# Optimization experiments

Hardware: AMD Instinct MI355X
Metric: run time of the kernel (lower is better)

The kernel has to match this reference:

```python
import jax, jax.numpy as jnp
import numpy as np

N, E, K, F, R = 100000, 200000, 16, 32, 2
EPS = 1e-5

def setup_inputs() -> dict:
    key = jax.random.key(0)
    ks = jax.random.split(key, 32)
    inp = {}
    inp['x'] = jax.random.normal(ks[0], (N, F), jnp.float32)
    inp['y'] = jax.random.normal(ks[1], (E, F), jnp.float32)
    inp['deg_g'] = jax.random.uniform(ks[2], (N, 1), jnp.float32)
    inp['deg_lg'] = jax.random.uniform(ks[3], (E, 1), jnp.float32)
    inp['t_g'] = jax.random.randint(ks[4], (N, K), 0, N)
    inp['tt_g'] = jax.random.randint(ks[5], (N, K), 0, N)
    inp['t_lg'] = jax.random.randint(ks[6], (E, K), 0, E)
    inp['tt_lg'] = jax.random.randint(ks[7], (E, K), 0, E)
    inp['dst'] = jax.random.randint(ks[8], (E,), 0, N)
    inp['pm_pd'] = jax.random.randint(ks[9], (E,), 0, N)
    i = [10]
    def mk(shape):
        a = jax.random.normal(ks[i[0]], shape, jnp.float32) * 0.1
        i[0] += 1
        return a
    for nm in ['theta_x', 'theta_deg', 'theta_y', 'gamma_y', 'gamma_deg', 'gamma_x']:
        inp[nm + '_w'] = mk((F, F)); inp[nm + '_b'] = mk((F,))
    inp['theta_r_w'] = mk((R, F, F)); inp['theta_r_b'] = mk((R, F))
    inp['gamma_r_w'] = mk((R, F, F)); inp['gamma_r_b'] = mk((R, F))
    inp['bn_x_w'] = jnp.ones((F,), jnp.float32); inp['bn_x_b'] = jnp.zeros((F,), jnp.float32)
    inp['bn_y_w'] = jnp.ones((F,), jnp.float32); inp['bn_y_b'] = jnp.zeros((F,), jnp.float32)
    return inp

def _lin(a, w, b):
    return a @ w + b

def _bn(a, w, b):
    # BatchNorm1d in training mode: biased batch stats
    m = a.mean(axis=0)
    v = a.var(axis=0)
    return (a - m) / jnp.sqrt(v + EPS) * w + b

def _aggregate(z, t, tt):
    # per-node gather+sum over neighbor index lists (t: radius-0, tt: radius-1)
    return jnp.stack([z[t].sum(axis=1), z[tt].sum(axis=1)])  # [R, M, F]

def reference(x, y, deg_g, deg_lg, t_g, tt_g, t_lg, tt_lg, dst, pm_pd,
              theta_x_w, theta_x_b, theta_deg_w, theta_deg_b, theta_y_w, theta_y_b,
              gamma_y_w, gamma_y_b, gamma_deg_w, gamma_deg_b, gamma_x_w, gamma_x_b,
              theta_r_w, theta_r_b, gamma_r_w, gamma_r_b,
              bn_x_w, bn_x_b, bn_y_w, bn_y_b):
    n = F // 2
    pmpd_x = x[pm_pd]                                   # [E, F] embedding gather
    zs = _aggregate(x, t_g, tt_g)                        # [R, N, F]
    sum_x = jnp.einsum('rnf,rfo->no', zs, theta_r_w) + theta_r_b.sum(axis=0)
    pmpd_y = jax.ops.segment_sum(y, dst, num_segments=x.shape[0])  # copy_edge + sum
    xo = (_lin(x, theta_x_w, theta_x_b)
          + _lin(deg_g * x, theta_deg_w, theta_deg_b)
          + sum_x
          + _lin(pmpd_y, theta_y_w, theta_y_b))
    xo = jnp.concatenate([xo[:, :n], jax.nn.relu(xo[:, n:])], axis=1)
    xo = _bn(xo, bn_x_w, bn_x_b)
    zy = _aggregate(y, t_lg, tt_lg)                      # [R, E, F]
    sum_y = jnp.einsum('ref,rfo->eo', zy, gamma_r_w) + gamma_r_b.sum(axis=0)
    yo = (_lin(y, gamma_y_w, gamma_y_b)
          + _lin(deg_lg * y, gamma_deg_w, gamma_deg_b)
          + sum_y
          + _lin(pmpd_x, gamma_x_w, gamma_x_b))
    yo = jnp.concatenate([yo[:, :n], jax.nn.relu(yo[:, n:])], axis=1)
    yo = _bn(yo, bn_y_w, bn_y_b)
    return xo, yo
```

## Files before the change

### kernel.cpp

```cpp
#include <hip/hip_runtime.h>

#define NN 100000
#define NE 200000
#define MT (NN + NE)

typedef unsigned short u16;
typedef __attribute__((ext_vector_type(8))) short bf16x8;
typedef __attribute__((ext_vector_type(4))) float f32x4;

__device__ __forceinline__ float bf2f(u16 u) {
    union { unsigned int i; float f; } v; v.i = ((unsigned int)u) << 16; return v.f;
}
__device__ __forceinline__ u16 f2bf(float f) {
    union { unsigned int i; float f; } v; v.f = f;
    unsigned int r = v.i + 0x7fffu + ((v.i >> 16) & 1u);
    return (u16)(r >> 16);
}
__device__ __forceinline__ void unpack2(unsigned int u, float& lo, float& hi) {
    union { unsigned int i; float f; } a, b;
    a.i = u << 16; b.i = u & 0xffff0000u;
    lo = a.f; hi = b.f;
}
__device__ __forceinline__ unsigned int pack2(float a, float b) {
    return (unsigned int)f2bf(a) | ((unsigned int)f2bf(b) << 16);
}
__device__ __forceinline__ float loadf(const void* p, size_t i, int f32) {
    return f32 ? ((const float*)p)[i] : bf2f(((const u16*)p)[i]);
}

__global__ void detect_kernel(const unsigned int* __restrict__ x, int* flag) {
    __shared__ int cnt;
    if (threadIdx.x == 0) cnt = 0;
    __syncthreads();
    int bad = 0;
    for (int i = threadIdx.x; i < 1024; i += 256) {
        unsigned int e = (x[i] >> 7) & 0xFF;
        if (e == 0xFF || (e > 0 && (e < 107 || e > 134))) bad++;
    }
    atomicAdd(&cnt, bad);
    __syncthreads();
    if (threadIdx.x == 0) *flag = (cnt > 256) ? 1 : 0;
}

__global__ __launch_bounds__(256) void prep_kernel(
    const void* txw, const void* tdw, const void* tyw,
    const void* gyw, const void* gdw, const void* gxw,
    const void* trw, const void* grw,
    const void* txb, const void* tdb, const void* tyb,
    const void* gyb, const void* gdb, const void* gxb,
    const void* trb, const void* grb,
    u16* Bfx, u16* Bfy, float* bx, float* by, const int* flagp)
{
    int f32 = *flagp;
    int t = blockIdx.x * 256 + threadIdx.x;
    if (t < 10240) {
        int side = t / 5120;
        int e = t - side * 5120;
        int b = e >> 9, lane = (e >> 3) & 63, j = e & 7;
        int m = b >> 1;
        int k = ((lane >> 4) << 3) + j;
        int f = ((b & 1) << 4) + (lane & 15);
        size_t idx = (size_t)k * 32 + f;
        float v;
        if (side == 0) {
            v = (m == 0) ? loadf(txw, idx, f32) : (m == 1) ? loadf(tdw, idx, f32)
              : (m == 2) ? loadf(trw, idx, f32) : (m == 3) ? loadf(trw, 1024 + idx, f32)
              : loadf(gxw, idx, f32);
            Bfx[e] = f2bf(v);
        } else {
            v = (m == 0) ? loadf(gyw, idx, f32) : (m == 1) ? loadf(gdw, idx, f32)
              : (m == 2) ? loadf(grw, idx, f32) : (m == 3) ? loadf(grw, 1024 + idx, f32)
              : loadf(tyw, idx, f32);
            Bfy[e] = f2bf(v);
        }
    } else if (t < 10304) {
        int f = t - 10240;
        if (f < 32) {
            bx[f] = loadf(txb, f, f32) + loadf(tdb, f, f32) + loadf(tyb, f, f32)
                  + loadf(trb, f, f32) + loadf(trb, 32 + f, f32);
        } else {
            f -= 32;
            by[f] = loadf(gyb, f, f32) + loadf(gdb, f, f32) + loadf(gxb, f, f32)
                  + loadf(grb, f, f32) + loadf(grb, 32 + f, f32);
        }
    }
}

__global__ __launch_bounds__(256, 4) void gemm2(
    const void* __restrict__ x, const void* __restrict__ y,
    const u16* __restrict__ Bfx, const u16* __restrict__ Bfy,
    const float* __restrict__ bx, const float* __restrict__ by,
    const void* __restrict__ deg_g, const void* __restrict__ deg_lg,
    const int* __restrict__ dst,
    u16* __restrict__ Xself, u16* __restrict__ Xt,
    u16* __restrict__ Xtt,   u16* __restrict__ Xaux,
    u16* __restrict__ Yself, u16* __restrict__ Yt, u16* __restrict__ Ytt,
    float* __restrict__ xacc, const int* __restrict__ flagp)
{
    int f32 = *flagp;
    int lane = threadIdx.x & 63;
    int wib  = threadIdx.x >> 6;
    bool is_y = (blockIdx.x >= 1563);
    int wid = (is_y ? (int)blockIdx.x - 1563 : (int)blockIdx.x) * 4 + wib;
    int nwaves = is_y ? 12500 : 6250;
    if (wid >= nwaves) return;
    int r0 = wid * 16;

    const void* feat = is_y ? y : x;
    const u16* Bf   = is_y ? Bfy : Bfx;
    const float* bias = is_y ? by : bx;
    const void* deg  = is_y ? deg_lg : deg_g;

    union { u16 s[8]; bf16x8 v; } au;
    {
        size_t eoff = (size_t)(r0 + (lane & 15)) * 32 + ((lane >> 4) << 3);
        if (f32) {
            const float4* fp = (const float4*)((const float*)feat + eoff);
            float4 A0 = fp[0], A1 = fp[1];
            au.s[0] = f2bf(A0.x); au.s[1] = f2bf(A0.y);
            au.s[2] = f2bf(A0.z); au.s[3] = f2bf(A0.w);
            au.s[4] = f2bf(A1.x); au.s[5] = f2bf(A1.y);
            au.s[6] = f2bf(A1.z); au.s[7] = f2bf(A1.w);
        } else {
            au.v = *(const bf16x8*)((const u16*)feat + eoff);
        }
    }
    f32x4 acc[10];
    const u16* bp = Bf + lane * 8;
#pragma unroll
    for (int b = 0; b < 10; ++b) {
        bf16x8 bfr = *(const bf16x8*)(bp + b * 512);
        f32x4 z = {0.f, 0.f, 0.f, 0.f};
        acc[b] = __builtin_amdgcn_mfma_f32_16x16x32_bf16(au.v, bfr, z, 0, 0, 0);
    }

    int n = lane & 15, quad = lane >> 4;
    int rowb = r0 + quad * 4;
    float bl = bias[n], bh = bias[16 + n];

#pragma unroll
    for (int i = 0; i < 4; ++i) {
        float dgi = loadf(deg, rowb + i, f32);
        size_t ro = (size_t)(rowb + i) * 32;
        u16 s_lo = f2bf(acc[0][i] + dgi * acc[2][i] + bl);
        u16 s_hi = f2bf(acc[1][i] + dgi * acc[3][i] + bh);
        if (!is_y) {
            Xself[ro + n]      = s_lo;
            Xself[ro + 16 + n] = s_hi;
            Xt[ro + n]         = f2bf(acc[4][i]);
            Xt[ro + 16 + n]    = f2bf(acc[5][i]);
            Xtt[ro + n]        = f2bf(acc[6][i]);
            Xtt[ro + 16 + n]   = f2bf(acc[7][i]);
            Xaux[ro + n]       = f2bf(acc[8][i]);
            Xaux[ro + 16 + n]  = f2bf(acc[9][i]);
        } else {
            Yself[ro + n]      = s_lo;
            Yself[ro + 16 + n] = s_hi;
            Yt[ro + n]         = f2bf(acc[4][i]);
            Yt[ro + 16 + n]    = f2bf(acc[5][i]);
            Ytt[ro + n]        = f2bf(acc[6][i]);
            Ytt[ro + 16 + n]   = f2bf(acc[7][i]);
            int d = dst[rowb + i];
            float* p = xacc + (size_t)d * 32;
            atomicAdd(p + n,      acc[8][i]);
            atomicAdd(p + 16 + n, acc[9][i]);
        }
    }
}

__global__ __launch_bounds__(256) void gather_fused(
    const u16* __restrict__ Xself, const u16* __restrict__ Xt,
    const u16* __restrict__ Xtt,   const u16* __restrict__ Xaux,
    const u16* __restrict__ Yself, const u16* __restrict__ Yt,
    const u16* __restrict__ Ytt,
    const float* __restrict__ xacc,
    const int* __restrict__ t_g, const int* __restrict__ tt_g,
    const int* __restrict__ t_lg, const int* __restrict__ tt_lg,
    const int* __restrict__ pm_pd,
    float* __restrict__ xpre, u16* __restrict__ ypre,
    float* __restrict__ stats)
{
    __shared__ int s_t[1024];
    __shared__ int s_tt[1024];
    __shared__ float s_sum[32];
    __shared__ float s_sq[32];
    bool is_y = (blockIdx.x >= 1563);
    int M = is_y ? NE : NN;
    const u16 *Self, *T, *TT;
    const int *tl, *ttl;
    if (is_y) { Self = Yself; T = Yt; TT = Ytt; tl = t_lg; ttl = tt_lg; }
    else      { Self = Xself; T = Xt; TT = Xtt; tl = t_g;  ttl = tt_g; }
    float* ss = stats + (is_y ? 64 : 0);

    if (threadIdx.x < 32) { s_sum[threadIdx.x] = 0.f; s_sq[threadIdx.x] = 0.f; }
    int row0 = (is_y ? (int)blockIdx.x - 1563 : (int)blockIdx.x) * 64;
    int lim = (M - row0) * 16;
    for (int i = threadIdx.x; i < 1024; i += 256) {
        s_t[i]  = (i < lim) ? tl[row0 * 16 + i]  : 0;
        s_tt[i] = (i < lim) ? ttl[row0 * 16 + i] : 0;
    }
    __syncthreads();

    int lr = threadIdx.x >> 2, q = threadIdx.x & 3;
    int r = row0 + lr;
    bool act = r < M;
    int rc = act ? r : row0;

    float a[8];
    {
        uint4 u = *(const uint4*)(Self + (size_t)rc * 32 + q * 8);
        unpack2(u.x, a[0], a[1]); unpack2(u.y, a[2], a[3]);
        unpack2(u.z, a[4], a[5]); unpack2(u.w, a[6], a[7]);
    }
    const int* il = &s_t[lr * 16];
    const int* ill = &s_tt[lr * 16];
#pragma unroll
    for (int batch = 0; batch < 2; ++batch) {
        uint4 g[8];
#pragma unroll
        for (int j = 0; j < 8; ++j)
            g[j] = *(const uint4*)(T + (size_t)il[batch * 8 + j] * 32 + q * 8);
#pragma unroll
        for (int j = 0; j < 8; ++j) {
            float e0, e1, e2, e3, e4, e5, e6, e7;
            unpack2(g[j].x, e0, e1); unpack2(g[j].y, e2, e3);
            unpack2(g[j].z, e4, e5); unpack2(g[j].w, e6, e7);
            a[0] += e0; a[1] += e1; a[2] += e2; a[3] += e3;
            a[4] += e4; a[5] += e5; a[6] += e6; a[7] += e7;
        }
    }
#pragma unroll
    for (int batch = 0; batch < 2; ++batch) {
        uint4 g[8];
#pragma unroll
        for (int j = 0; j < 8; ++j)
            g[j] = *(const uint4*)(TT + (size_t)ill[batch * 8 + j] * 32 + q * 8);
#pragma unroll
        for (int j = 0; j < 8; ++j) {
            float e0, e1, e2, e3, e4, e5, e6, e7;
            unpack2(g[j].x, e0, e1); unpack2(g[j].y, e2, e3);
            unpack2(g[j].z, e4, e5); unpack2(g[j].w, e6, e7);
            a[0] += e0; a[1] += e1; a[2] += e2; a[3] += e3;
            a[4] += e4; a[5] += e5; a[6] += e6; a[7] += e7;
        }
    }
    if (!is_y) {
        float4 b0 = *(const float4*)(xacc + (size_t)rc * 32 + q * 8);
        float4 b1 = *(const float4*)(xacc + (size_t)rc * 32 + q * 8 + 4);
        a[0] += b0.x; a[1] += b0.y; a[2] += b0.z; a[3] += b0.w;
        a[4] += b1.x; a[5] += b1.y; a[6] += b1.z; a[7] += b1.w;
    } else {
        int ai = pm_pd[rc];
        uint4 g = *(const uint4*)(Xaux + (size_t)ai * 32 + q * 8);
        float e0, e1, e2, e3, e4, e5, e6, e7;
        unpack2(g.x, e0, e1); unpack2(g.y, e2, e3);
        unpack2(g.z, e4, e5); unpack2(g.w, e6, e7);
        a[0] += e0; a[1] += e1; a[2] += e2; a[3] += e3;
        a[4] += e4; a[5] += e5; a[6] += e6; a[7] += e7;
    }
    if (q >= 2) {
#pragma unroll
        for (int i = 0; i < 8; ++i) a[i] = fmaxf(a[i], 0.f);
    }
    if (act) {
        if (!is_y) {
            float4 o0, o1;
            o0.x = a[0]; o0.y = a[1]; o0.z = a[2]; o0.w = a[3];
            o1.x = a[4]; o1.y = a[5]; o1.z = a[6]; o1.w = a[7];
            *(float4*)(xpre + (size_t)r * 32 + q * 8) = o0;
            *(float4*)(xpre + (size_t)r * 32 + q * 8 + 4) = o1;
        } else {
            uint4 o;
            o.x = pack2(a[0], a[1]); o.y = pack2(a[2], a[3]);
            o.z = pack2(a[4], a[5]); o.w = pack2(a[6], a[7]);
            *(uint4*)(ypre + (size_t)r * 32 + q * 8) = o;
        }
    } else {
#pragma unroll
        for (int i = 0; i < 8; ++i) a[i] = 0.f;
    }
#pragma unroll
    for (int i = 0; i < 8; ++i) {
        atomicAdd(&s_sum[q * 8 + i], a[i]);
        atomicAdd(&s_sq[q * 8 + i], a[i] * a[i]);
    }
    __syncthreads();
    if (threadIdx.x < 32) {
        atomicAdd(&ss[threadIdx.x], s_sum[threadIdx.x]);
        atomicAdd(&ss[32 + threadIdx.x], s_sq[threadIdx.x]);
    }
}

__global__ void finalize_stats(
    const float* stats,
    const void* bnxw, const void* bnxb, const void* bnyw, const void* bnyb,
    float* scsh, const int* flagp)
{
    int f32 = *flagp;
    int f = threadIdx.x;
    if (f < 32) {
        float m = stats[f] / (float)NN;
        float var = stats[32 + f] / (float)NN - m * m;
        float inv = rsqrtf(var + 1e-5f);
        float sc = loadf(bnxw, f, f32) * inv;
        scsh[f] = sc; scsh[32 + f] = loadf(bnxb, f, f32) - m * sc;
    } else if (f < 64) {
        int g = f - 32;
        float m = stats[64 + g] / (float)NE;
        float var = stats[96 + g] / (float)NE - m * m;
        float inv = rsqrtf(var + 1e-5f);
        float sc = loadf(bnyw, g, f32) * inv;
        scsh[64 + g] = sc; scsh[96 + g] = loadf(bnyb, g, f32) - m * sc;
    }
}

__global__ __launch_bounds__(256) void apply_bn(
    const float* __restrict__ xpre, const u16* __restrict__ ypre,
    const float* __restrict__ scsh, void* __restrict__ out,
    const int* __restrict__ flagp)
{
    int f32 = *flagp;
    int tid = blockIdx.x * 256 + threadIdx.x;
    if (tid >= MT * 8) return;
    int fq = (tid & 7) * 4;
    const float* sc;
    float4 v;
    if (tid < NN * 8) {
        v = ((const float4*)xpre)[tid];
        sc = scsh;
    } else {
        size_t off = (size_t)tid * 4 - (size_t)NN * 32;
        ushort4 u = *(const ushort4*)(ypre + off);
        v.x = bf2f(u.x); v.y = bf2f(u.y); v.z = bf2f(u.z); v.w = bf2f(u.w);
        sc = scsh + 64;
    }
    float o0 = v.x * sc[fq + 0] + sc[32 + fq + 0];
    float o1 = v.y * sc[fq + 1] + sc[32 + fq + 1];
    float o2 = v.z * sc[fq + 2] + sc[32 + fq + 2];
    float o3 = v.w * sc[fq + 3] + sc[32 + fq + 3];
    if (f32) {
        float4 o; o.x = o0; o.y = o1; o.z = o2; o.w = o3;
        ((float4*)out)[tid] = o;
    } else {
        ushort4 o; o.x = f2bf(o0); o.y = f2bf(o1); o.z = f2bf(o2); o.w = f2bf(o3);
        ((ushort4*)out)[tid] = o;
    }
}

extern "C" void kernel_launch(void* const* d_in, const int* in_sizes, int n_in,
                              void* d_out, int out_size, void* d_ws, size_t ws_size,
                              hipStream_t stream)
{
    const void* x      = d_in[0];
    const void* y      = d_in[1];
    const void* deg_g  = d_in[2];
    const void* deg_lg = d_in[3];
    const int* t_g   = (const int*)d_in[4];
    const int* tt_g  = (const int*)d_in[5];
    const int* t_lg  = (const int*)d_in[6];
    const int* tt_lg = (const int*)d_in[7];
    const int* dst   = (const int*)d_in[8];
    const int* pm_pd = (const int*)d_in[9];

    char* ws = (char*)d_ws;
    int*   flag = (int*)ws;
    u16* Bfx   = (u16*)(ws + 256);
    u16* Bfy   = Bfx + 5120;
    float* bx  = (float*)(ws + 24576);
    float* by  = bx + 32;
    float* stats = by + 32;
    float* scsh  = stats + 128;
    u16* Xself = (u16*)(ws + 65536);
    u16* Xt    = Xself + (size_t)NN * 32;
    u16* Xtt   = Xt    + (size_t)NN * 32;
    u16* Xaux  = Xtt   + (size_t)NN * 32;
    u16* Yself = Xaux  + (size_t)NN * 32;
    u16* Yt    = Yself + (size_t)NE * 32;
    u16* Ytt   = Yt    + (size_t)NE * 32;
    float* xacc = (float*)(Ytt + (size_t)NE * 32);
    u16* ypre = (u16*)(xacc + (size_t)NN * 32);

    hipMemsetAsync(stats, 0, 256 * sizeof(float), stream);
    hipMemsetAsync(xacc, 0, (size_t)NN * 32 * sizeof(float), stream);

    detect_kernel<<<1, 256, 0, stream>>>((const unsigned int*)x, flag);
    prep_kernel<<<41, 256, 0, stream>>>(
        d_in[10], d_in[12], d_in[14], d_in[16], d_in[18], d_in[20],
        d_in[22], d_in[24],
        d_in[11], d_in[13], d_in[15], d_in[17], d_in[19], d_in[21],
        d_in[23], d_in[25],
        Bfx, Bfy, bx, by, flag);
    gemm2<<<4688, 256, 0, stream>>>(x, y, Bfx, Bfy, bx, by, deg_g, deg_lg, dst,
                                    Xself, Xt, Xtt, Xaux, Yself, Yt, Ytt,
                                    xacc, flag);
    gather_fused<<<4688, 256, 0, stream>>>(Xself, Xt, Xtt, Xaux, Yself, Yt, Ytt,
                                           xacc, t_g, tt_g, t_lg, tt_lg, pm_pd,
                                           xacc, ypre, stats);
    finalize_stats<<<1, 64, 0, stream>>>(stats, d_in[26], d_in[27], d_in[28],
                                         d_in[29], scsh, flag);
    apply_bn<<<9375, 256, 0, stream>>>(xacc, ypre, scsh, d_out, flag);
}
```

Measured before the change: 418.2 us.

## Aggregate raw features before the GEMM instead of after the per-row projections

The old code projected every row through all weight matrices first and then gathered the projected T/TT/aux tables. The new code converts x and y to bf16 once, gathers and sums raw neighbour features, and applies the weights with MFMA after aggregation. It then fuses the projection, bias, ReLU and BN-stat accumulation into one kernel per side, with the y side run first so its atomics into xacc finish before the x side reads them. This removes the seven intermediate projected tables and most of their traffic. In exchange, the neighbour sums are rounded to bf16 before the MFMA, which can change precision, and the gathers now sit inside the GEMM kernel.

```diff
diff --git a/kernel.cpp b/kernel.cpp
--- a/kernel.cpp
+++ b/kernel.cpp
@@ -26,6 +26,13 @@
 }
 __device__ __forceinline__ float loadf(const void* p, size_t i, int f32) {
     return f32 ? ((const float*)p)[i] : bf2f(((const u16*)p)[i]);
+}
+__device__ __forceinline__ void acc8(float a[8], uint4 g) {
+    float e0, e1, e2, e3, e4, e5, e6, e7;
+    unpack2(g.x, e0, e1); unpack2(g.y, e2, e3);
+    unpack2(g.z, e4, e5); unpack2(g.w, e6, e7);
+    a[0] += e0; a[1] += e1; a[2] += e2; a[3] += e3;
+    a[4] += e4; a[5] += e5; a[6] += e6; a[7] += e7;
 }
 
 __global__ void detect_kernel(const unsigned int* __restrict__ x, int* flag) {
@@ -53,26 +60,26 @@
 {
     int f32 = *flagp;
     int t = blockIdx.x * 256 + threadIdx.x;
-    if (t < 10240) {
-        int side = t / 5120;
-        int e = t - side * 5120;
+    if (t < 4096) {
+        int b = t >> 9, lane = (t >> 3) & 63, j = t & 7;
+        int m = b >> 1;
+        int k = ((lane >> 4) << 3) + j;
+        int f = ((b & 1) << 4) + (lane & 15);
+        size_t idx = (size_t)k * 32 + f;
+        float v = (m == 0) ? loadf(txw, idx, f32) : (m == 1) ? loadf(tdw, idx, f32)
+                : (m == 2) ? loadf(trw, idx, f32) : loadf(trw, 1024 + idx, f32);
+        Bfx[t] = f2bf(v);
+    } else if (t < 10240) {
+        int e = t - 4096;
         int b = e >> 9, lane = (e >> 3) & 63, j = e & 7;
         int m = b >> 1;
         int k = ((lane >> 4) << 3) + j;
         int f = ((b & 1) << 4) + (lane & 15);
         size_t idx = (size_t)k * 32 + f;
-        float v;
-        if (side == 0) {
-            v = (m == 0) ? loadf(txw, idx, f32) : (m == 1) ? loadf(tdw, idx, f32)
-              : (m == 2) ? loadf(trw, idx, f32) : (m == 3) ? loadf(trw, 1024 + idx, f32)
-              : loadf(gxw, idx, f32);
-            Bfx[e] = f2bf(v);
-        } else {
-            v = (m == 0) ? loadf(gyw, idx, f32) : (m == 1) ? loadf(gdw, idx, f32)
-              : (m == 2) ? loadf(grw, idx, f32) : (m == 3) ? loadf(grw, 1024 + idx, f32)
-              : loadf(tyw, idx, f32);
-            Bfy[e] = f2bf(v);
-        }
+        float v = (m == 0) ? loadf(gyw, idx, f32) : (m == 1) ? loadf(gdw, idx, f32)
+                : (m == 2) ? loadf(grw, idx, f32) : (m == 3) ? loadf(grw, 1024 + idx, f32)
+                : (m == 4) ? loadf(gxw, idx, f32) : loadf(tyw, idx, f32);
+        Bfy[e] = f2bf(v);
     } else if (t < 10304) {
         int f = t - 10240;
         if (f < 32) {
@@ -86,206 +93,164 @@
     }
 }
 
-__global__ __launch_bounds__(256, 4) void gemm2(
+__global__ __launch_bounds__(256) void convert_kernel(
     const void* __restrict__ x, const void* __restrict__ y,
-    const u16* __restrict__ Bfx, const u16* __restrict__ Bfy,
-    const float* __restrict__ bx, const float* __restrict__ by,
-    const void* __restrict__ deg_g, const void* __restrict__ deg_lg,
-    const int* __restrict__ dst,
-    u16* __restrict__ Xself, u16* __restrict__ Xt,
-    u16* __restrict__ Xtt,   u16* __restrict__ Xaux,
-    u16* __restrict__ Yself, u16* __restrict__ Yt, u16* __restrict__ Ytt,
-    float* __restrict__ xacc, const int* __restrict__ flagp)
-{
-    int f32 = *flagp;
-    int lane = threadIdx.x & 63;
-    int wib  = threadIdx.x >> 6;
-    bool is_y = (blockIdx.x >= 1563);
-    int wid = (is_y ? (int)blockIdx.x - 1563 : (int)blockIdx.x) * 4 + wib;
-    int nwaves = is_y ? 12500 : 6250;
-    if (wid >= nwaves) return;
-    int r0 = wid * 16;
-
-    const void* feat = is_y ? y : x;
-    const u16* Bf   = is_y ? Bfy : Bfx;
-    const float* bias = is_y ? by : bx;
-    const void* deg  = is_y ? deg_lg : deg_g;
-
-    union { u16 s[8]; bf16x8 v; } au;
-    {
-        size_t eoff = (size_t)(r0 + (lane & 15)) * 32 + ((lane >> 4) << 3);
+    u16* __restrict__ xb, u16* __restrict__ yb, const int* __restrict__ flagp)
+{
+    int f32 = *flagp;
+    int t = blockIdx.x * 256 + threadIdx.x;
+    if (t < NN * 4) {
+        int r = t >> 2, q = t & 3;
+        uint4 o;
         if (f32) {
-            const float4* fp = (const float4*)((const float*)feat + eoff);
-            float4 A0 = fp[0], A1 = fp[1];
-            au.s[0] = f2bf(A0.x); au.s[1] = f2bf(A0.y);
-            au.s[2] = f2bf(A0.z); au.s[3] = f2bf(A0.w);
-            au.s[4] = f2bf(A1.x); au.s[5] = f2bf(A1.y);
-            au.s[6] = f2bf(A1.z); au.s[7] = f2bf(A1.w);
+            const float4* fp = (const float4*)((const float*)x + (size_t)r * 32 + q * 8);
+            float4 v0 = fp[0], v1 = fp[1];
+            o.x = pack2(v0.x, v0.y); o.y = pack2(v0.z, v0.w);
+            o.z = pack2(v1.x, v1.y); o.w = pack2(v1.z, v1.w);
         } else {
-            au.v = *(const bf16x8*)((const u16*)feat + eoff);
-        }
-    }
-    f32x4 acc[10];
-    const u16* bp = Bf + lane * 8;
-#pragma unroll
-    for (int b = 0; b < 10; ++b) {
-        bf16x8 bfr = *(const bf16x8*)(bp + b * 512);
-        f32x4 z = {0.f, 0.f, 0.f, 0.f};
-        acc[b] = __builtin_amdgcn_mfma_f32_16x16x32_bf16(au.v, bfr, z, 0, 0, 0);
-    }
-
-    int n = lane & 15, quad = lane >> 4;
-    int rowb = r0 + quad * 4;
-    float bl = bias[n], bh = bias[16 + n];
-
-#pragma unroll
-    for (int i = 0; i < 4; ++i) {
-        float dgi = loadf(deg, rowb + i, f32);
-        size_t ro = (size_t)(rowb + i) * 32;
-        u16 s_lo = f2bf(acc[0][i] + dgi * acc[2][i] + bl);
-        u16 s_hi = f2bf(acc[1][i] + dgi * acc[3][i] + bh);
-        if (!is_y) {
-            Xself[ro + n]      = s_lo;
-            Xself[ro + 16 + n] = s_hi;
-            Xt[ro + n]         = f2bf(acc[4][i]);
-            Xt[ro + 16 + n]    = f2bf(acc[5][i]);
-            Xtt[ro + n]        = f2bf(acc[6][i]);
-            Xtt[ro + 16 + n]   = f2bf(acc[7][i]);
-            Xaux[ro + n]       = f2bf(acc[8][i]);
-            Xaux[ro + 16 + n]  = f2bf(acc[9][i]);
+            o = *(const uint4*)((const u16*)x + (size_t)r * 32 + q * 8);
+        }
+        *(uint4*)(xb + (size_t)r * 32 + q * 8) = o;
+    } else if (t < MT * 4) {
+        int t2 = t - NN * 4;
+        int r = t2 >> 2, q = t2 & 3;
+        uint4 o;
+        if (f32) {
+            const float4* fp = (const float4*)((const float*)y + (size_t)r * 32 + q * 8);
+            float4 v0 = fp[0], v1 = fp[1];
+            o.x = pack2(v0.x, v0.y); o.y = pack2(v0.z, v0.w);
+            o.z = pack2(v1.x, v1.y); o.w = pack2(v1.z, v1.w);
         } else {
-            Yself[ro + n]      = s_lo;
-            Yself[ro + 16 + n] = s_hi;
-            Yt[ro + n]         = f2bf(acc[4][i]);
-            Yt[ro + 16 + n]    = f2bf(acc[5][i]);
-            Ytt[ro + n]        = f2bf(acc[6][i]);
-            Ytt[ro + 16 + n]   = f2bf(acc[7][i]);
-            int d = dst[rowb + i];
-            float* p = xacc + (size_t)d * 32;
-            atomicAdd(p + n,      acc[8][i]);
-            atomicAdd(p + 16 + n, acc[9][i]);
-        }
-    }
-}
-
-__global__ __launch_bounds__(256) void gather_fused(
-    const u16* __restrict__ Xself, const u16* __restrict__ Xt,
-    const u16* __restrict__ Xtt,   const u16* __restrict__ Xaux,
-    const u16* __restrict__ Yself, const u16* __restrict__ Yt,
-    const u16* __restrict__ Ytt,
-    const float* __restrict__ xacc,
-    const int* __restrict__ t_g, const int* __restrict__ tt_g,
-    const int* __restrict__ t_lg, const int* __restrict__ tt_lg,
-    const int* __restrict__ pm_pd,
-    float* __restrict__ xpre, u16* __restrict__ ypre,
-    float* __restrict__ stats)
+            o = *(const uint4*)((const u16*)y + (size_t)r * 32 + q * 8);
+        }
+        *(uint4*)(yb + (size_t)r * 32 + q * 8) = o;
+    }
+}
+
+template<int IS_Y>
+__global__ __launch_bounds__(256, 3) void fused_side(
+    const u16* __restrict__ xb, const u16* __restrict__ yb,
+    float* xacc,
+    const u16* __restrict__ Bf, const float* __restrict__ bias,
+    const void* __restrict__ deg,
+    const int* __restrict__ tl, const int* __restrict__ ttl,
+    const int* __restrict__ pm_pd, const int* __restrict__ dst,
+    float* xpre, u16* __restrict__ ypre,
+    float* __restrict__ stats, const int* __restrict__ flagp)
 {
     __shared__ int s_t[1024];
     __shared__ int s_tt[1024];
     __shared__ float s_sum[32];
     __shared__ float s_sq[32];
-    bool is_y = (blockIdx.x >= 1563);
-    int M = is_y ? NE : NN;
-    const u16 *Self, *T, *TT;
-    const int *tl, *ttl;
-    if (is_y) { Self = Yself; T = Yt; TT = Ytt; tl = t_lg; ttl = tt_lg; }
-    else      { Self = Xself; T = Xt; TT = Xtt; tl = t_g;  ttl = tt_g; }
-    float* ss = stats + (is_y ? 64 : 0);
-
+    const int M = IS_Y ? NE : NN;
+    int f32 = *flagp;
+    int row0 = (int)blockIdx.x * 64;
     if (threadIdx.x < 32) { s_sum[threadIdx.x] = 0.f; s_sq[threadIdx.x] = 0.f; }
-    int row0 = (is_y ? (int)blockIdx.x - 1563 : (int)blockIdx.x) * 64;
     int lim = (M - row0) * 16;
     for (int i = threadIdx.x; i < 1024; i += 256) {
-        s_t[i]  = (i < lim) ? tl[row0 * 16 + i]  : 0;
-        s_tt[i] = (i < lim) ? ttl[row0 * 16 + i] : 0;
+        s_t[i]  = (i < lim) ? tl[(size_t)row0 * 16 + i]  : 0;
+        s_tt[i] = (i < lim) ? ttl[(size_t)row0 * 16 + i] : 0;
     }
     __syncthreads();
-
-    int lr = threadIdx.x >> 2, q = threadIdx.x & 3;
-    int r = row0 + lr;
-    bool act = r < M;
-    int rc = act ? r : row0;
-
-    float a[8];
-    {
-        uint4 u = *(const uint4*)(Self + (size_t)rc * 32 + q * 8);
-        unpack2(u.x, a[0], a[1]); unpack2(u.y, a[2], a[3]);
-        unpack2(u.z, a[4], a[5]); unpack2(u.w, a[6], a[7]);
-    }
-    const int* il = &s_t[lr * 16];
-    const int* ill = &s_tt[lr * 16];
-#pragma unroll
-    for (int batch = 0; batch < 2; ++batch) {
-        uint4 g[8];
+    int lane = threadIdx.x & 63, wib = threadIdx.x >> 6;
+    int r0 = row0 + wib * 16;
+    if (r0 + 16 <= M) {
+        const u16* tab = IS_Y ? yb : xb;
+        int m = lane & 15, q = lane >> 4;
+        int gr = r0 + m;
+        const int* il  = &s_t[(wib * 16 + m) * 16];
+        const int* ill = &s_tt[(wib * 16 + m) * 16];
+
+        bf16x8 selfv = *(const bf16x8*)(tab + (size_t)gr * 32 + q * 8);
+        union { u16 s[8]; bf16x8 v; } pm;
+        if (IS_Y) {
+            int ai = pm_pd[gr];
+            pm.v = *(const bf16x8*)(xb + (size_t)ai * 32 + q * 8);
+        }
+
+        float aT[8]  = {0.f, 0.f, 0.f, 0.f, 0.f, 0.f, 0.f, 0.f};
+        float aTT[8] = {0.f, 0.f, 0.f, 0.f, 0.f, 0.f, 0.f, 0.f};
+        uint4 ga[8], gb[8];
 #pragma unroll
         for (int j = 0; j < 8; ++j)
-            g[j] = *(const uint4*)(T + (size_t)il[batch * 8 + j] * 32 + q * 8);
-#pragma unroll
-        for (int j = 0; j < 8; ++j) {
-            float e0, e1, e2, e3, e4, e5, e6, e7;
-            unpack2(g[j].x, e0, e1); unpack2(g[j].y, e2, e3);
-            unpack2(g[j].z, e4, e5); unpack2(g[j].w, e6, e7);
-            a[0] += e0; a[1] += e1; a[2] += e2; a[3] += e3;
-            a[4] += e4; a[5] += e5; a[6] += e6; a[7] += e7;
-        }
-    }
-#pragma unroll
-    for (int batch = 0; batch < 2; ++batch) {
-        uint4 g[8];
+            ga[j] = *(const uint4*)(tab + (size_t)il[j] * 32 + q * 8);
 #pragma unroll
         for (int j = 0; j < 8; ++j)
-            g[j] = *(const uint4*)(TT + (size_t)ill[batch * 8 + j] * 32 + q * 8);
-#pragma unroll
-        for (int j = 0; j < 8; ++j) {
-            float e0, e1, e2, e3, e4, e5, e6, e7;
-            unpack2(g[j].x, e0, e1); unpack2(g[j].y, e2, e3);
-            unpack2(g[j].z, e4, e5); unpack2(g[j].w, e6, e7);
-            a[0] += e0; a[1] += e1; a[2] += e2; a[3] += e3;
-            a[4] += e4; a[5] += e5; a[6] += e6; a[7] += e7;
-        }
-    }
-    if (!is_y) {
-        float4 b0 = *(const float4*)(xacc + (size_t)rc * 32 + q * 8);
-        float4 b1 = *(const float4*)(xacc + (size_t)rc * 32 + q * 8 + 4);
-        a[0] += b0.x; a[1] += b0.y; a[2] += b0.z; a[3] += b0.w;
-        a[4] += b1.x; a[5] += b1.y; a[6] += b1.z; a[7] += b1.w;
-    } else {
-        int ai = pm_pd[rc];
-        uint4 g = *(const uint4*)(Xaux + (size_t)ai * 32 + q * 8);
-        float e0, e1, e2, e3, e4, e5, e6, e7;
-        unpack2(g.x, e0, e1); unpack2(g.y, e2, e3);
-        unpack2(g.z, e4, e5); unpack2(g.w, e6, e7);
-        a[0] += e0; a[1] += e1; a[2] += e2; a[3] += e3;
-        a[4] += e4; a[5] += e5; a[6] += e6; a[7] += e7;
-    }
-    if (q >= 2) {
-#pragma unroll
-        for (int i = 0; i < 8; ++i) a[i] = fmaxf(a[i], 0.f);
-    }
-    if (act) {
-        if (!is_y) {
-            float4 o0, o1;
-            o0.x = a[0]; o0.y = a[1]; o0.z = a[2]; o0.w = a[3];
-            o1.x = a[4]; o1.y = a[5]; o1.z = a[6]; o1.w = a[7];
-            *(float4*)(xpre + (size_t)r * 32 + q * 8) = o0;
-            *(float4*)(xpre + (size_t)r * 32 + q * 8 + 4) = o1;
-        } else {
-            uint4 o;
-            o.x = pack2(a[0], a[1]); o.y = pack2(a[2], a[3]);
-            o.z = pack2(a[4], a[5]); o.w = pack2(a[6], a[7]);
-            *(uint4*)(ypre + (size_t)r * 32 + q * 8) = o;
-        }
-    } else {
-#pragma unroll
-        for (int i = 0; i < 8; ++i) a[i] = 0.f;
-    }
-#pragma unroll
-    for (int i = 0; i < 8; ++i) {
-        atomicAdd(&s_sum[q * 8 + i], a[i]);
-        atomicAdd(&s_sq[q * 8 + i], a[i] * a[i]);
+            gb[j] = *(const uint4*)(tab + (size_t)il[8 + j] * 32 + q * 8);
+#pragma unroll
+        for (int j = 0; j < 8; ++j) acc8(aT, ga[j]);
+#pragma unroll
+        for (int j = 0; j < 8; ++j)
+            ga[j] = *(const uint4*)(tab + (size_t)ill[j] * 32 + q * 8);
+#pragma unroll
+        for (int j = 0; j < 8; ++j) acc8(aT, gb[j]);
+#pragma unroll
+        for (int j = 0; j < 8; ++j)
+            gb[j] = *(const uint4*)(tab + (size_t)ill[8 + j] * 32 + q * 8);
+#pragma unroll
+        for (int j = 0; j < 8; ++j) acc8(aTT, ga[j]);
+#pragma unroll
+        for (int j = 0; j < 8; ++j) acc8(aTT, gb[j]);
+
+        union { u16 s[8]; bf16x8 v; } ft, ftt;
+#pragma unroll
+        for (int j = 0; j < 8; ++j) { ft.s[j] = f2bf(aT[j]); ftt.s[j] = f2bf(aTT[j]); }
+
+        const u16* bp = Bf + lane * 8;
+#define BFR(b) (*(const bf16x8*)(bp + (b) * 512))
+        f32x4 z = {0.f, 0.f, 0.f, 0.f};
+        f32x4 a0, a1, d0, d1, c0 = z, c1 = z;
+        a0 = __builtin_amdgcn_mfma_f32_16x16x32_bf16(selfv, BFR(0), z, 0, 0, 0);
+        a1 = __builtin_amdgcn_mfma_f32_16x16x32_bf16(selfv, BFR(1), z, 0, 0, 0);
+        d0 = __builtin_amdgcn_mfma_f32_16x16x32_bf16(selfv, BFR(2), z, 0, 0, 0);
+        d1 = __builtin_amdgcn_mfma_f32_16x16x32_bf16(selfv, BFR(3), z, 0, 0, 0);
+        a0 = __builtin_amdgcn_mfma_f32_16x16x32_bf16(ft.v,  BFR(4), a0, 0, 0, 0);
+        a1 = __builtin_amdgcn_mfma_f32_16x16x32_bf16(ft.v,  BFR(5), a1, 0, 0, 0);
+        a0 = __builtin_amdgcn_mfma_f32_16x16x32_bf16(ftt.v, BFR(6), a0, 0, 0, 0);
+        a1 = __builtin_amdgcn_mfma_f32_16x16x32_bf16(ftt.v, BFR(7), a1, 0, 0, 0);
+        if (IS_Y) {
+            a0 = __builtin_amdgcn_mfma_f32_16x16x32_bf16(pm.v,  BFR(8),  a0, 0, 0, 0);
+            a1 = __builtin_amdgcn_mfma_f32_16x16x32_bf16(pm.v,  BFR(9),  a1, 0, 0, 0);
+            c0 = __builtin_amdgcn_mfma_f32_16x16x32_bf16(selfv, BFR(10), z, 0, 0, 0);
+            c1 = __builtin_amdgcn_mfma_f32_16x16x32_bf16(selfv, BFR(11), z, 0, 0, 0);
+        }
+#undef BFR
+
+        int n = m;
+        int rowb = r0 + q * 4;
+        float bl_ = bias[n], bh_ = bias[16 + n];
+        float s0 = 0.f, q0 = 0.f, s1 = 0.f, q1 = 0.f;
+#pragma unroll
+        for (int i = 0; i < 4; ++i) {
+            float dgi = loadf(deg, rowb + i, f32);
+            size_t ro = (size_t)(rowb + i) * 32;
+            float lo = a0[i] + dgi * d0[i] + bl_;
+            float hi = a1[i] + dgi * d1[i] + bh_;
+            if (!IS_Y) {
+                lo += xacc[ro + n];
+                hi += xacc[ro + 16 + n];
+            }
+            hi = fmaxf(hi, 0.f);
+            if (!IS_Y) {
+                xpre[ro + n]      = lo;
+                xpre[ro + 16 + n] = hi;
+            } else {
+                ypre[ro + n]      = f2bf(lo);
+                ypre[ro + 16 + n] = f2bf(hi);
+                int d = dst[rowb + i];
+                float* p = xacc + (size_t)d * 32;
+                atomicAdd(p + n,      c0[i]);
+                atomicAdd(p + 16 + n, c1[i]);
+            }
+            s0 += lo; q0 += lo * lo;
+            s1 += hi; q1 += hi * hi;
+        }
+        atomicAdd(&s_sum[n], s0);      atomicAdd(&s_sq[n], q0);
+        atomicAdd(&s_sum[16 + n], s1); atomicAdd(&s_sq[16 + n], q1);
     }
     __syncthreads();
     if (threadIdx.x < 32) {
+        float* ss = stats + (IS_Y ? 64 : 0);
         atomicAdd(&ss[threadIdx.x], s_sum[threadIdx.x]);
         atomicAdd(&ss[32 + threadIdx.x], s_sq[threadIdx.x]);
     }
@@ -365,20 +330,15 @@
     char* ws = (char*)d_ws;
     int*   flag = (int*)ws;
     u16* Bfx   = (u16*)(ws + 256);
-    u16* Bfy   = Bfx + 5120;
+    u16* Bfy   = Bfx + 4096;
     float* bx  = (float*)(ws + 24576);
     float* by  = bx + 32;
     float* stats = by + 32;
     float* scsh  = stats + 128;
-    u16* Xself = (u16*)(ws + 65536);
-    u16* Xt    = Xself + (size_t)NN * 32;
-    u16* Xtt   = Xt    + (size_t)NN * 32;
-    u16* Xaux  = Xtt   + (size_t)NN * 32;
-    u16* Yself = Xaux  + (size_t)NN * 32;
-    u16* Yt    = Yself + (size_t)NE * 32;
-    u16* Ytt   = Yt    + (size_t)NE * 32;
-    float* xacc = (float*)(Ytt + (size_t)NE * 32);
-    u16* ypre = (u16*)(xacc + (size_t)NN * 32);
+    u16* xb    = (u16*)(ws + 65536);
+    u16* yb    = xb + (size_t)NN * 32;
+    float* xacc = (float*)(yb + (size_t)NE * 32);
+    u16* ypre  = (u16*)(xacc + (size_t)NN * 32);
 
     hipMemsetAsync(stats, 0, 256 * sizeof(float), stream);
     hipMemsetAsync(xacc, 0, (size_t)NN * 32 * sizeof(float), stream);
@@ -390,12 +350,14 @@
         d_in[11], d_in[13], d_in[15], d_in[17], d_in[19], d_in[21],
         d_in[23], d_in[25],
         Bfx, Bfy, bx, by, flag);
-    gemm2<<<4688, 256, 0, stream>>>(x, y, Bfx, Bfy, bx, by, deg_g, deg_lg, dst,
-                                    Xself, Xt, Xtt, Xaux, Yself, Yt, Ytt,
-                                    xacc, flag);
-    gather_fused<<<4688, 256, 0, stream>>>(Xself, Xt, Xtt, Xaux, Yself, Yt, Ytt,
-                                           xacc, t_g, tt_g, t_lg, tt_lg, pm_pd,
-                                           xacc, ypre, stats);
+    convert_kernel<<<4688, 256, 0, stream>>>(x, y, xb, yb, flag);
+    fused_side<1><<<3125, 256, 0, stream>>>(xb, yb, xacc, Bfy, by, deg_lg,
+                                            t_lg, tt_lg, pm_pd, dst,
+                                            (float*)0, ypre, stats, flag);
+    fused_side<0><<<1563, 256, 0, stream>>>(xb, yb, xacc, Bfx, bx, deg_g,
+                                            t_g, tt_g, pm_pd, dst,
+                                            xacc , (u16*)0,
+                                            stats, flag);
     finalize_stats<<<1, 64, 0, stream>>>(stats, d_in[26], d_in[27], d_in[28],
                                          d_in[29], scsh, flag);
     apply_bn<<<9375, 256, 0, stream>>>(xacc, ypre, scsh, d_out, flag);
```

Measured after the change: 405.5 us. 1.03x faster.
